# Performance work log

Hardware: AMD Instinct MI355X
Metric: run time of the kernel (lower is better)

## Reference

```python
import jax, jax.numpy as jnp
import numpy as np

DIM = 512
HEAD_DIM = 32
NUM_HEADS = DIM // HEAD_DIM
SCALE = HEAD_DIM ** -0.5
SPARSE_WINDOW = 64
LN_EPS = 1e-5


def setup_inputs() -> dict:
    key = jax.random.key(0)
    ks = jax.random.split(key, 7)
    B, S = 2, 2048
    x = jax.random.normal(ks[0], (B, S, DIM), dtype=jnp.float32)
    # parameters (Linear weights stored as [in, out] for x @ W)
    W_qkv = jax.random.normal(ks[1], (DIM, 2 * DIM), dtype=jnp.float32) * (DIM ** -0.5)
    b_qkv = jnp.zeros((2 * DIM,), dtype=jnp.float32)
    W_out = jax.random.normal(ks[2], (DIM, DIM), dtype=jnp.float32) * (DIM ** -0.5)
    b_out = jnp.zeros((DIM,), dtype=jnp.float32)
    ln_gamma = jnp.ones((DIM,), dtype=jnp.float32)
    ln_beta = jnp.zeros((DIM,), dtype=jnp.float32)
    return {"x": x, "W_qkv": W_qkv, "b_qkv": b_qkv, "W_out": W_out,
            "b_out": b_out, "ln_gamma": ln_gamma, "ln_beta": ln_beta}


def _attn(x, W_qkv, b_qkv, W_out, b_out, ln_gamma, ln_beta):
    B, S, _ = x.shape
    qkv = x @ W_qkv + b_qkv                        # [B,S,2*DIM]
    qk, v = qkv[..., :DIM], qkv[..., DIM:]
    q = jax.nn.silu(qk) * SCALE                    # shared-projection nonlinear Q
    k = jnp.tanh(qk)                               # shared-projection nonlinear K
    q = q.reshape(B, S, NUM_HEADS, HEAD_DIM)
    k = k.reshape(B, S, NUM_HEADS, HEAD_DIM)
    v = v.reshape(B, S, NUM_HEADS, HEAD_DIM)
    scores = jnp.einsum('bihd,bjhd->bhij', q, k)   # [B,H,S,S]
    # sparse window: MULTIPLICATIVE zeroing outside |i-j|<=w (faithful to source)
    i = jnp.arange(S)
    band = (jnp.abs(i[:, None] - i[None, :]) <= SPARSE_WINDOW).astype(scores.dtype)
    scores = scores * band                         # zeros still enter softmax as exp(0)
    probs = jax.nn.softmax(scores, axis=-1)
    out = jnp.einsum('bhij,bjhd->bihd', probs, v).reshape(B, S, DIM)
    out = out @ W_out + b_out
    y = x + out                                    # residual (dropout is eval no-op)
    mu = jnp.mean(y, axis=-1, keepdims=True)
    var = jnp.var(y, axis=-1, keepdims=True)
    return (y - mu) * jax.lax.rsqrt(var + LN_EPS) * ln_gamma + ln_beta


def reference(x, W_qkv, b_qkv, W_out, b_out, ln_gamma, ln_beta):
    return _attn(x, W_qkv, b_qkv, W_out, b_out, ln_gamma, ln_beta)
```

## Files before the change

### kernel.cpp

```cpp
#include <hip/hip_runtime.h>
#include <cstdint>
#include <cstddef>

#define DIMX 512
#define HDIM 32
#define NHEADS 16
#define SEQ 2048
#define BATCH 2
#define MTOT (BATCH*SEQ)
#define WIN 64
#define QSCALE 0.17677669529663687f

typedef __bf16 bf16x8 __attribute__((ext_vector_type(8)));
typedef float f32x4 __attribute__((ext_vector_type(4)));

__device__ __forceinline__ unsigned short f2bf(float f){
  unsigned u = __builtin_bit_cast(unsigned, f);
  u += 0x7FFFu + ((u >> 16) & 1u);
  return (unsigned short)(u >> 16);
}
__device__ __forceinline__ float bf2f(unsigned short s){
  return __builtin_bit_cast(float, ((unsigned)s) << 16);
}
__device__ __forceinline__ unsigned pk(float a, float b){
  return (unsigned)f2bf(a) | ((unsigned)f2bf(b) << 16);
}

__device__ __forceinline__ void gl_lds16(const void* g, void* l){
  __builtin_amdgcn_global_load_lds(
      (const __attribute__((address_space(1))) unsigned*)g,
      (__attribute__((address_space(3))) unsigned*)(unsigned)(unsigned long long)l,
      16, 0, 0);
}

template<int N> __device__ __forceinline__ void vmwait(){
  if      constexpr (N ==  8) asm volatile("s_waitcnt vmcnt(8)"  ::: "memory");
  else if constexpr (N ==  4) asm volatile("s_waitcnt vmcnt(4)"  ::: "memory");
  else                        asm volatile("s_waitcnt vmcnt(0)"  ::: "memory");
}

__global__ void k_prep(const float* __restrict__ x, unsigned short* __restrict__ xb,
                       const float* __restrict__ Wq, unsigned short* __restrict__ Wqt,
                       const float* __restrict__ Wo, unsigned short* __restrict__ Wot){
  int bx = blockIdx.x;
  if (bx < 1024){
    int i = bx * 256 + threadIdx.x;
    const float4* p = (const float4*)x + (size_t)i * 2;
    float4 a = p[0], b = p[1];
    uint4 o;
    o.x = pk(a.x, a.y); o.y = pk(a.z, a.w);
    o.z = pk(b.x, b.y); o.w = pk(b.z, b.w);
    ((uint4*)xb)[i] = o;
    return;
  }
  __shared__ float tile[32][33];
  int i = bx - 1024;
  int bxx = i % 48, byy = i / 48;
  const float* W; unsigned short* Wt; int N, n0;
  if (bxx < 32){ W = Wq; Wt = Wqt; N = 1024; n0 = bxx * 32; }
  else         { W = Wo; Wt = Wot; N = 512;  n0 = (bxx - 32) * 32; }
  int k0 = byy * 32;
  int tx = threadIdx.x & 31, ty = threadIdx.x >> 5;
  #pragma unroll
  for (int r = 0; r < 32; r += 8)
    tile[ty + r][tx] = W[(size_t)(k0 + ty + r) * N + n0 + tx];
  __syncthreads();
  #pragma unroll
  for (int r = 0; r < 32; r += 8)
    Wt[(size_t)(n0 + ty + r) * 512 + k0 + tx] = f2bf(tile[tx][ty + r]);
}

template<int MODE, int BM, int BN, int NBN>
__launch_bounds__(256)
__global__ void k_gemm(const unsigned short* __restrict__ A,
                       const unsigned short* __restrict__ Bt,
                       const float* __restrict__ bias,
                       unsigned short* __restrict__ qb,
                       unsigned short* __restrict__ kb,
                       unsigned short* __restrict__ vt,
                       float* __restrict__ vsum_p,
                       const unsigned short* __restrict__ xb,
                       unsigned short* __restrict__ yb)
{
  const int K = 512;
  constexpr int NWG = (MTOT / BM) * NBN;
  constexpr int MF  = BM / 32, NF = BN / 32;
  constexpr int LPS = (BM + BN) / 32;
  __shared__ __align__(16) unsigned short lds[2][(BM + BN) * 64];
  int tid = threadIdx.x;
  int wid = tid >> 6, lane = tid & 63;
  int wm = wid >> 1, wn = wid & 1;
  int lane15 = lane & 15, laneh = lane >> 4;

  int g = blockIdx.x;
  int gwi = (g & 7) * (NWG / 8) + (g >> 3);
  int bm = gwi / NBN, bn = gwi % NBN;

  f32x4 acc[MF][NF] = {};

  int srow_off = lane >> 3;
  int spos     = lane & 7;

  auto STAGE = [&](int buf, int kt){
    int k0 = kt * 64;
    #pragma unroll
    for (int c = 0; c < MF; ++c){
      int cidx = wid * MF + c;
      int r = cidx * 8 + srow_off;
      int ch = spos ^ (r & 7);
      gl_lds16(A + (size_t)(bm * BM + r) * K + k0 + ch * 8, &lds[buf][cidx * 512]);
    }
    #pragma unroll
    for (int c = 0; c < NF; ++c){
      int cidx = wid * NF + c;
      int r = cidx * 8 + srow_off;
      int ch = spos ^ (r & 7);
      gl_lds16(Bt + (size_t)(bn * BN + r) * K + k0 + ch * 8, &lds[buf][BM * 64 + cidx * 512]);
    }
  };

  auto COMPUTE = [&](int buf){
    #pragma unroll
    for (int kh = 0; kh < 2; ++kh){
      int chunk = kh * 4 + laneh;
      bf16x8 af[MF], bfv[NF];
      #pragma unroll
      for (int mi = 0; mi < MF; ++mi){
        int row = wm * (BM / 2) + mi * 16 + lane15;
        af[mi] = *(const bf16x8*)&lds[buf][row * 64 + (chunk ^ (row & 7)) * 8];
      }
      #pragma unroll
      for (int ni = 0; ni < NF; ++ni){
        int row = wn * (BN / 2) + ni * 16 + lane15;
        bfv[ni] = *(const bf16x8*)&lds[buf][BM * 64 + row * 64 + (chunk ^ (row & 7)) * 8];
      }
      #pragma unroll
      for (int mi = 0; mi < MF; ++mi)
        #pragma unroll
        for (int ni = 0; ni < NF; ++ni)
          acc[mi][ni] = __builtin_amdgcn_mfma_f32_16x16x32_bf16(af[mi], bfv[ni], acc[mi][ni], 0, 0, 0);
    }
  };

  STAGE(0, 0);
  #pragma unroll
  for (int kt = 0; kt < 8; ++kt){
    if (kt < 7) STAGE((kt + 1) & 1, kt + 1);
    if (kt < 7) vmwait<LPS>(); else vmwait<0>();
    __builtin_amdgcn_s_barrier();
    __builtin_amdgcn_sched_barrier(0);
    COMPUTE(kt & 1);
    __builtin_amdgcn_s_barrier();
    __builtin_amdgcn_sched_barrier(0);
  }

  if (MODE == 0 && bn >= 4){
    unsigned short (*tp)[136] = (unsigned short (*)[136])&lds[0][0];
    #pragma unroll
    for (int mi = 0; mi < MF; ++mi)
      #pragma unroll
      for (int ni = 0; ni < NF; ++ni)
        #pragma unroll
        for (int r = 0; r < 4; ++r){
          int ml = wm * (BM / 2) + mi * 16 + laneh * 4 + r;
          int nl = wn * (BN / 2) + ni * 16 + lane15;
          tp[nl][ml] = f2bf(acc[mi][ni][r] + bias[bn * BN + nl]);
        }
    __syncthreads();
    int nl = tid >> 1, half = tid & 1;
    int h = (bn - 4) * 4 + (nl >> 5), d = nl & 31;
    int b = bm >> 4, sc = bm & 15;
    int bh = b * 16 + h;
    uint4 v4[8];
    float ssum = 0.f;
    #pragma unroll
    for (int p = 0; p < 8; ++p){
      v4[p] = *(const uint4*)&tp[nl][half * 64 + p * 8];
      const unsigned* w = (const unsigned*)&v4[p];
      #pragma unroll
      for (int j = 0; j < 4; ++j)
        ssum += bf2f((unsigned short)(w[j] & 0xffff)) + bf2f((unsigned short)(w[j] >> 16));
    }
    ssum += __shfl_xor(ssum, 1);
    size_t vtoff = (size_t)(bh * HDIM + d) * SEQ + sc * 128 + half * 64;
    #pragma unroll
    for (int p = 0; p < 8; ++p) *(uint4*)(vt + vtoff + p * 8) = v4[p];
    if (half == 0) vsum_p[(sc * 32 + bh) * HDIM + d] = ssum;
  } else {
    #pragma unroll
    for (int mi = 0; mi < MF; ++mi){
      #pragma unroll
      for (int ni = 0; ni < NF; ++ni){
        #pragma unroll
        for (int r = 0; r < 4; ++r){
          int m = bm * BM + wm * (BM / 2) + mi * 16 + laneh * 4 + r;
          int nloc = wn * (BN / 2) + ni * 16 + lane15;
          int n = bn * BN + nloc;
          float val = acc[mi][ni][r] + bias[n];
          if (MODE == 0){
            int b = m >> 11, s = m & 2047;
            int h = n >> 5, d = n & 31;
            size_t idx = ((size_t)(b * 16 + h) * SEQ + s) * HDIM + d;
            float sv = val / (1.0f + __expf(-val)) * QSCALE;
            float tv = 1.0f - 2.0f / (1.0f + __expf(2.0f * val));
            qb[idx] = f2bf(sv);
            kb[idx] = f2bf(tv);
          } else {
            size_t idx = (size_t)m * DIMX + n;
            yb[idx] = f2bf(val + bf2f(xb[idx]));
          }
        }
      }
    }
  }
}

__launch_bounds__(256)
__global__ void k_attn(const unsigned short* __restrict__ qb,
                       const unsigned short* __restrict__ kb,
                       const unsigned short* __restrict__ vt,
                       const float* __restrict__ vsum_p,
                       unsigned short* __restrict__ ao)
{
  __shared__ unsigned short p_lds[4][16][40];
  int tid = threadIdx.x, wid = tid >> 6, lane = tid & 63;
  int lane15 = lane & 15, laneh = lane >> 4;
  int bh = blockIdx.y, b = bh >> 4, h = bh & 15;
  int s0 = blockIdx.x * 64 + wid * 16;

  bf16x8 qf = *(const bf16x8*)(qb + ((size_t)bh * SEQ + s0 + lane15) * HDIM + laneh * 8);
  float vs0 = 0.f, vs1 = 0.f;
  #pragma unroll
  for (int c = 0; c < 16; ++c){
    vs0 += vsum_p[(c * 32 + bh) * HDIM + lane15];
    vs1 += vsum_p[(c * 32 + bh) * HDIM + 16 + lane15];
  }

  f32x4 accv[2] = {};
  float dsum[4] = {0.f, 0.f, 0.f, 0.f};

  for (int jt = 0; jt < 9; ++jt){
    int j0 = s0 - 64 + jt * 16;
    int jc = min(max(j0 + lane15, 0), SEQ - 1);
    bf16x8 kf = *(const bf16x8*)(kb + ((size_t)bh * SEQ + jc) * HDIM + laneh * 8);
    f32x4 z = {0.f, 0.f, 0.f, 0.f};
    f32x4 sv = __builtin_amdgcn_mfma_f32_16x16x32_bf16(qf, kf, z, 0, 0, 0);
    #pragma unroll
    for (int r = 0; r < 4; ++r){
      int i = s0 + laneh * 4 + r;
      int j = j0 + lane15;
      int dj = i - j;
      bool inb = (dj <= WIN) && (dj >= -WIN) && (j >= 0) && (j < SEQ);
      float w = inb ? (__expf(sv[r]) - 1.0f) : 0.0f;
      dsum[r] += w;
      p_lds[wid][laneh * 4 + r][(jt & 1) * 16 + lane15] = f2bf(w);
    }
    if (jt & 1){
      int jc0 = j0 - 16;
      bf16x8 pa = *(const bf16x8*)&p_lds[wid][lane15][laneh * 8];
      int jv = min(max(jc0 + laneh * 8, 0), SEQ - 8);
      bf16x8 v0 = *(const bf16x8*)(vt + (size_t)(bh * HDIM + lane15) * SEQ + jv);
      bf16x8 v1 = *(const bf16x8*)(vt + (size_t)(bh * HDIM + 16 + lane15) * SEQ + jv);
      accv[0] = __builtin_amdgcn_mfma_f32_16x16x32_bf16(pa, v0, accv[0], 0, 0, 0);
      accv[1] = __builtin_amdgcn_mfma_f32_16x16x32_bf16(pa, v1, accv[1], 0, 0, 0);
    }
  }
  {
    #pragma unroll
    for (int r = 0; r < 4; ++r)
      p_lds[wid][laneh * 4 + r][16 + lane15] = 0;
    int jc0 = s0 + 64;
    bf16x8 pa = *(const bf16x8*)&p_lds[wid][lane15][laneh * 8];
    int jv = min(max(jc0 + laneh * 8, 0), SEQ - 8);
    bf16x8 v0 = *(const bf16x8*)(vt + (size_t)(bh * HDIM + lane15) * SEQ + jv);
    bf16x8 v1 = *(const bf16x8*)(vt + (size_t)(bh * HDIM + 16 + lane15) * SEQ + jv);
    accv[0] = __builtin_amdgcn_mfma_f32_16x16x32_bf16(pa, v0, accv[0], 0, 0, 0);
    accv[1] = __builtin_amdgcn_mfma_f32_16x16x32_bf16(pa, v1, accv[1], 0, 0, 0);
  }

  #pragma unroll
  for (int r = 0; r < 4; ++r){
    float v = dsum[r];
    v += __shfl_xor(v, 1); v += __shfl_xor(v, 2);
    v += __shfl_xor(v, 4); v += __shfl_xor(v, 8);
    dsum[r] = v;
  }
  #pragma unroll
  for (int r = 0; r < 4; ++r){
    int i = s0 + laneh * 4 + r;
    float dn = (float)SEQ + dsum[r];
    float o0 = (accv[0][r] + vs0) / dn;
    float o1 = (accv[1][r] + vs1) / dn;
    size_t base = (size_t)(b * SEQ + i) * DIMX + h * HDIM;
    ao[base + lane15]      = f2bf(o0);
    ao[base + 16 + lane15] = f2bf(o1);
  }
}

__global__ void k_ln(const unsigned short* __restrict__ yb, const float* __restrict__ gamma,
                     const float* __restrict__ beta, float* __restrict__ out){
  int wid = threadIdx.x >> 6, lane = threadIdx.x & 63;
  int row = blockIdx.x * 4 + wid;
  uint4 u = *(const uint4*)(yb + (size_t)row * DIMX + lane * 8);
  const unsigned* w = (const unsigned*)&u;
  float v[8];
  #pragma unroll
  for (int j = 0; j < 4; ++j){
    v[2*j]   = bf2f((unsigned short)(w[j] & 0xffff));
    v[2*j+1] = bf2f((unsigned short)(w[j] >> 16));
  }
  float s = 0.f, ss = 0.f;
  #pragma unroll
  for (int j = 0; j < 8; ++j){ s += v[j]; ss += v[j] * v[j]; }
  #pragma unroll
  for (int m = 1; m < 64; m <<= 1){ s += __shfl_xor(s, m); ss += __shfl_xor(ss, m); }
  float mu = s * (1.f / DIMX);
  float var = ss * (1.f / DIMX) - mu * mu;
  float inv = rsqrtf(var + 1e-5f);
  float4 g0 = *(const float4*)(gamma + lane * 8);
  float4 g1 = *(const float4*)(gamma + lane * 8 + 4);
  float4 b0 = *(const float4*)(beta + lane * 8);
  float4 b1 = *(const float4*)(beta + lane * 8 + 4);
  float4 o0, o1;
  o0.x = (v[0] - mu) * inv * g0.x + b0.x; o0.y = (v[1] - mu) * inv * g0.y + b0.y;
  o0.z = (v[2] - mu) * inv * g0.z + b0.z; o0.w = (v[3] - mu) * inv * g0.w + b0.w;
  o1.x = (v[4] - mu) * inv * g1.x + b1.x; o1.y = (v[5] - mu) * inv * g1.y + b1.y;
  o1.z = (v[6] - mu) * inv * g1.z + b1.z; o1.w = (v[7] - mu) * inv * g1.w + b1.w;
  float* op = out + (size_t)row * DIMX + lane * 8;
  *(float4*)op = o0; *(float4*)(op + 4) = o1;
}

extern "C" void kernel_launch(void* const* d_in, const int* in_sizes, int n_in,
                              void* d_out, int out_size, void* d_ws, size_t ws_size,
                              hipStream_t stream){
  const float* x      = (const float*)d_in[0];
  const float* W_qkv  = (const float*)d_in[1];
  const float* b_qkv  = (const float*)d_in[2];
  const float* W_out  = (const float*)d_in[3];
  const float* b_out  = (const float*)d_in[4];
  const float* gamma  = (const float*)d_in[5];
  const float* beta   = (const float*)d_in[6];
  float* out = (float*)d_out;

  char* ws = (char*)d_ws;
  size_t off = 0;
  auto alloc = [&](size_t bytes){ void* p = ws + off; off += (bytes + 255) & ~(size_t)255; return p; };
  unsigned short* xb  = (unsigned short*)alloc((size_t)MTOT * DIMX * 2);
  unsigned short* wqt = (unsigned short*)alloc((size_t)1024 * 512 * 2);
  unsigned short* wot = (unsigned short*)alloc((size_t)512 * 512 * 2);
  unsigned short* qb  = (unsigned short*)alloc((size_t)MTOT * DIMX * 2);
  unsigned short* kb  = (unsigned short*)alloc((size_t)MTOT * DIMX * 2);
  unsigned short* vt  = (unsigned short*)alloc((size_t)32 * HDIM * SEQ * 2);
  float*          vsm = (float*)alloc((size_t)16 * 32 * HDIM * 4);
  unsigned short* ao  = (unsigned short*)alloc((size_t)MTOT * DIMX * 2);
  unsigned short* yb  = (unsigned short*)alloc((size_t)MTOT * DIMX * 2);

  k_prep<<<1792, 256, 0, stream>>>(x, xb, W_qkv, wqt, W_out, wot);
  k_gemm<0, 128, 128, 8><<<256, 256, 0, stream>>>(xb, wqt, b_qkv, qb, kb, vt, vsm, nullptr, nullptr);
  k_attn<<<dim3(32, 32), 256, 0, stream>>>(qb, kb, vt, vsm, ao);
  k_gemm<1, 64, 64, 8><<<512, 256, 0, stream>>>(ao, wot, b_out, nullptr, nullptr, nullptr, nullptr, xb, yb);
  k_ln  <<<MTOT / 4, 256, 0, stream>>>(yb, gamma, beta, out);
}
```

Baseline: 45.03 us.

## Fuse output projection, residual add and LayerNorm into one kernel

Replaces the output-projection GEMM and the separate LayerNorm kernel with a single kernel. Each 512-thread block computes 16 full rows of ao@W_out with MFMA, stages the result in LDS, adds bias and residual, and normalizes in place. W_out is pre-packed in k_prep into the MFMA B-fragment layout so lanes load it directly from global memory without LDS staging. This drops one launch and the bf16 y round-trip through memory, at the cost of only 256 blocks, each streaming the whole W_out from L2 with no double buffering.

```diff
diff --git a/kernel.cpp b/kernel.cpp
--- a/kernel.cpp
+++ b/kernel.cpp
@@ -41,7 +41,7 @@
 
 __global__ void k_prep(const float* __restrict__ x, unsigned short* __restrict__ xb,
                        const float* __restrict__ Wq, unsigned short* __restrict__ Wqt,
-                       const float* __restrict__ Wo, unsigned short* __restrict__ Wot){
+                       const float* __restrict__ Wo, unsigned short* __restrict__ WotP){
   int bx = blockIdx.x;
   if (bx < 1024){
     int i = bx * 256 + threadIdx.x;
@@ -53,24 +53,42 @@
     ((uint4*)xb)[i] = o;
     return;
   }
-  __shared__ float tile[32][33];
-  int i = bx - 1024;
-  int bxx = i % 48, byy = i / 48;
-  const float* W; unsigned short* Wt; int N, n0;
-  if (bxx < 32){ W = Wq; Wt = Wqt; N = 1024; n0 = bxx * 32; }
-  else         { W = Wo; Wt = Wot; N = 512;  n0 = (bxx - 32) * 32; }
-  int k0 = byy * 32;
-  int tx = threadIdx.x & 31, ty = threadIdx.x >> 5;
-  #pragma unroll
-  for (int r = 0; r < 32; r += 8)
-    tile[ty + r][tx] = W[(size_t)(k0 + ty + r) * N + n0 + tx];
-  __syncthreads();
-  #pragma unroll
-  for (int r = 0; r < 32; r += 8)
-    Wt[(size_t)(n0 + ty + r) * 512 + k0 + tx] = f2bf(tile[tx][ty + r]);
-}
-
-template<int MODE, int BM, int BN, int NBN>
+  if (bx < 1536){
+    __shared__ float tile[32][33];
+    int i = bx - 1024;
+    int n0 = (i & 31) * 32, k0 = (i >> 5) * 32;
+    int tx = threadIdx.x & 31, ty = threadIdx.x >> 5;
+    #pragma unroll
+    for (int r = 0; r < 32; r += 8)
+      tile[ty + r][tx] = Wq[(size_t)(k0 + ty + r) * 1024 + n0 + tx];
+    __syncthreads();
+    #pragma unroll
+    for (int r = 0; r < 32; r += 8)
+      Wqt[(size_t)(n0 + ty + r) * 512 + k0 + tx] = f2bf(tile[tx][ty + r]);
+    return;
+  }
+  int wid = threadIdx.x >> 6, lane = threadIdx.x & 63;
+  int lane15 = lane & 15, laneh = lane >> 4;
+  int pair = (bx - 1536) * 4 + wid;
+  int nt = pair >> 3, ks = pair & 7;
+  int n = nt * 16 + lane15;
+  #pragma unroll
+  for (int kh = 0; kh < 2; ++kh){
+    int k0 = ks * 64 + kh * 32 + laneh * 8;
+    unsigned short pc[8];
+    #pragma unroll
+    for (int j = 0; j < 8; ++j)
+      pc[j] = f2bf(Wo[(size_t)(k0 + j) * 512 + n]);
+    uint4 o;
+    o.x = (unsigned)pc[0] | ((unsigned)pc[1] << 16);
+    o.y = (unsigned)pc[2] | ((unsigned)pc[3] << 16);
+    o.z = (unsigned)pc[4] | ((unsigned)pc[5] << 16);
+    o.w = (unsigned)pc[6] | ((unsigned)pc[7] << 16);
+    ((uint4*)WotP)[((size_t)(nt * 8 + ks) * 2 + kh) * 64 + lane] = o;
+  }
+}
+
+template<int BM, int BN, int NBN>
 __launch_bounds__(256)
 __global__ void k_gemm(const unsigned short* __restrict__ A,
                        const unsigned short* __restrict__ Bt,
@@ -78,9 +96,7 @@
                        unsigned short* __restrict__ qb,
                        unsigned short* __restrict__ kb,
                        unsigned short* __restrict__ vt,
-                       float* __restrict__ vsum_p,
-                       const unsigned short* __restrict__ xb,
-                       unsigned short* __restrict__ yb)
+                       float* __restrict__ vsum_p)
 {
   const int K = 512;
   constexpr int NWG = (MTOT / BM) * NBN;
@@ -154,7 +170,7 @@
     __builtin_amdgcn_sched_barrier(0);
   }
 
-  if (MODE == 0 && bn >= 4){
+  if (bn >= 4){
     unsigned short (*tp)[136] = (unsigned short (*)[136])&lds[0][0];
     #pragma unroll
     for (int mi = 0; mi < MF; ++mi)
@@ -194,21 +210,15 @@
         #pragma unroll
         for (int r = 0; r < 4; ++r){
           int m = bm * BM + wm * (BM / 2) + mi * 16 + laneh * 4 + r;
-          int nloc = wn * (BN / 2) + ni * 16 + lane15;
-          int n = bn * BN + nloc;
+          int n = bn * BN + wn * (BN / 2) + ni * 16 + lane15;
           float val = acc[mi][ni][r] + bias[n];
-          if (MODE == 0){
-            int b = m >> 11, s = m & 2047;
-            int h = n >> 5, d = n & 31;
-            size_t idx = ((size_t)(b * 16 + h) * SEQ + s) * HDIM + d;
-            float sv = val / (1.0f + __expf(-val)) * QSCALE;
-            float tv = 1.0f - 2.0f / (1.0f + __expf(2.0f * val));
-            qb[idx] = f2bf(sv);
-            kb[idx] = f2bf(tv);
-          } else {
-            size_t idx = (size_t)m * DIMX + n;
-            yb[idx] = f2bf(val + bf2f(xb[idx]));
-          }
+          int b = m >> 11, s = m & 2047;
+          int h = n >> 5, d = n & 31;
+          size_t idx = ((size_t)(b * 16 + h) * SEQ + s) * HDIM + d;
+          float sv = val / (1.0f + __expf(-val)) * QSCALE;
+          float tv = 1.0f - 2.0f / (1.0f + __expf(2.0f * val));
+          qb[idx] = f2bf(sv);
+          kb[idx] = f2bf(tv);
         }
       }
     }
@@ -297,37 +307,83 @@
   }
 }
 
-__global__ void k_ln(const unsigned short* __restrict__ yb, const float* __restrict__ gamma,
-                     const float* __restrict__ beta, float* __restrict__ out){
-  int wid = threadIdx.x >> 6, lane = threadIdx.x & 63;
-  int row = blockIdx.x * 4 + wid;
-  uint4 u = *(const uint4*)(yb + (size_t)row * DIMX + lane * 8);
-  const unsigned* w = (const unsigned*)&u;
-  float v[8];
-  #pragma unroll
-  for (int j = 0; j < 4; ++j){
-    v[2*j]   = bf2f((unsigned short)(w[j] & 0xffff));
-    v[2*j+1] = bf2f((unsigned short)(w[j] >> 16));
-  }
-  float s = 0.f, ss = 0.f;
-  #pragma unroll
-  for (int j = 0; j < 8; ++j){ s += v[j]; ss += v[j] * v[j]; }
-  #pragma unroll
-  for (int m = 1; m < 64; m <<= 1){ s += __shfl_xor(s, m); ss += __shfl_xor(ss, m); }
-  float mu = s * (1.f / DIMX);
+__launch_bounds__(512)
+__global__ void k_oln(const unsigned short* __restrict__ ao,
+                      const unsigned short* __restrict__ wotP,
+                      const float* __restrict__ bout,
+                      const unsigned short* __restrict__ xb,
+                      const float* __restrict__ gamma,
+                      const float* __restrict__ beta,
+                      float* __restrict__ out)
+{
+  __shared__ __align__(16) unsigned short asA[16 * 520];
+  __shared__ float tp[16][516];
+  int tid = threadIdx.x;
+  int wid = tid >> 6, lane = tid & 63;
+  int lane15 = lane & 15, laneh = lane >> 4;
+  int mrow0 = blockIdx.x * 16;
+
+  #pragma unroll
+  for (int c = 0; c < 2; ++c){
+    int row = wid * 2 + c;
+    gl_lds16(ao + (size_t)(mrow0 + row) * DIMX + (lane ^ (row & 7)) * 8,
+             &asA[row * 520]);
+  }
+
+  f32x4 acc[4] = {};
+  const uint4* bp = (const uint4*)wotP;
+
+  __syncthreads();
+
+  #pragma unroll
+  for (int kt = 0; kt < 8; ++kt){
+    #pragma unroll
+    for (int kh = 0; kh < 2; ++kh){
+      int ck = kt * 8 + kh * 4 + laneh;
+      bf16x8 af = *(const bf16x8*)&asA[lane15 * 520 + ((ck ^ (lane15 & 7)) * 8)];
+      #pragma unroll
+      for (int ni = 0; ni < 4; ++ni){
+        uint4 braw = bp[((size_t)((wid * 4 + ni) * 8 + kt) * 2 + kh) * 64 + lane];
+        acc[ni] = __builtin_amdgcn_mfma_f32_16x16x32_bf16(
+                     af, __builtin_bit_cast(bf16x8, braw), acc[ni], 0, 0, 0);
+      }
+    }
+  }
+
+  #pragma unroll
+  for (int ni = 0; ni < 4; ++ni){
+    int col = wid * 64 + ni * 16 + lane15;
+    float bv = bout[col];
+    #pragma unroll
+    for (int r = 0; r < 4; ++r)
+      tp[laneh * 4 + r][col] = acc[ni][r] + bv;
+  }
+  __syncthreads();
+
+  int tr = tid >> 5, seg = tid & 31;
+  const unsigned short* xr = xb + (size_t)(mrow0 + tr) * DIMX + seg * 16;
+  uint4 x0 = *(const uint4*)xr, x1 = *(const uint4*)(xr + 8);
+  unsigned xwv[8];
+  *(uint4*)&xwv[0] = x0; *(uint4*)&xwv[4] = x1;
+  float v[16], s = 0.f, ss = 0.f;
+  #pragma unroll
+  for (int j = 0; j < 16; ++j){
+    unsigned wb = xwv[j >> 1];
+    unsigned short hv = (j & 1) ? (unsigned short)(wb >> 16) : (unsigned short)(wb & 0xffff);
+    v[j] = tp[tr][seg * 16 + j] + bf2f(hv);
+    s += v[j]; ss += v[j] * v[j];
+  }
+  #pragma unroll
+  for (int m = 1; m < 32; m <<= 1){ s += __shfl_xor(s, m); ss += __shfl_xor(ss, m); }
+  float mu  = s * (1.f / DIMX);
   float var = ss * (1.f / DIMX) - mu * mu;
   float inv = rsqrtf(var + 1e-5f);
-  float4 g0 = *(const float4*)(gamma + lane * 8);
-  float4 g1 = *(const float4*)(gamma + lane * 8 + 4);
-  float4 b0 = *(const float4*)(beta + lane * 8);
-  float4 b1 = *(const float4*)(beta + lane * 8 + 4);
-  float4 o0, o1;
-  o0.x = (v[0] - mu) * inv * g0.x + b0.x; o0.y = (v[1] - mu) * inv * g0.y + b0.y;
-  o0.z = (v[2] - mu) * inv * g0.z + b0.z; o0.w = (v[3] - mu) * inv * g0.w + b0.w;
-  o1.x = (v[4] - mu) * inv * g1.x + b1.x; o1.y = (v[5] - mu) * inv * g1.y + b1.y;
-  o1.z = (v[6] - mu) * inv * g1.z + b1.z; o1.w = (v[7] - mu) * inv * g1.w + b1.w;
-  float* op = out + (size_t)row * DIMX + lane * 8;
-  *(float4*)op = o0; *(float4*)(op + 4) = o1;
+  float* op = out + (size_t)(mrow0 + tr) * DIMX + seg * 16;
+  const float* gp = gamma + seg * 16;
+  const float* bb = beta  + seg * 16;
+  #pragma unroll
+  for (int j = 0; j < 16; ++j)
+    op[j] = (v[j] - mu) * inv * gp[j] + bb[j];
 }
 
 extern "C" void kernel_launch(void* const* d_in, const int* in_sizes, int n_in,
@@ -345,19 +401,17 @@
   char* ws = (char*)d_ws;
   size_t off = 0;
   auto alloc = [&](size_t bytes){ void* p = ws + off; off += (bytes + 255) & ~(size_t)255; return p; };
-  unsigned short* xb  = (unsigned short*)alloc((size_t)MTOT * DIMX * 2);
-  unsigned short* wqt = (unsigned short*)alloc((size_t)1024 * 512 * 2);
-  unsigned short* wot = (unsigned short*)alloc((size_t)512 * 512 * 2);
-  unsigned short* qb  = (unsigned short*)alloc((size_t)MTOT * DIMX * 2);
-  unsigned short* kb  = (unsigned short*)alloc((size_t)MTOT * DIMX * 2);
-  unsigned short* vt  = (unsigned short*)alloc((size_t)32 * HDIM * SEQ * 2);
-  float*          vsm = (float*)alloc((size_t)16 * 32 * HDIM * 4);
-  unsigned short* ao  = (unsigned short*)alloc((size_t)MTOT * DIMX * 2);
-  unsigned short* yb  = (unsigned short*)alloc((size_t)MTOT * DIMX * 2);
-
-  k_prep<<<1792, 256, 0, stream>>>(x, xb, W_qkv, wqt, W_out, wot);
-  k_gemm<0, 128, 128, 8><<<256, 256, 0, stream>>>(xb, wqt, b_qkv, qb, kb, vt, vsm, nullptr, nullptr);
+  unsigned short* xb   = (unsigned short*)alloc((size_t)MTOT * DIMX * 2);
+  unsigned short* wqt  = (unsigned short*)alloc((size_t)1024 * 512 * 2);
+  unsigned short* wotP = (unsigned short*)alloc((size_t)512 * 512 * 2);
+  unsigned short* qb   = (unsigned short*)alloc((size_t)MTOT * DIMX * 2);
+  unsigned short* kb   = (unsigned short*)alloc((size_t)MTOT * DIMX * 2);
+  unsigned short* vt   = (unsigned short*)alloc((size_t)32 * HDIM * SEQ * 2);
+  float*          vsm  = (float*)alloc((size_t)16 * 32 * HDIM * 4);
+  unsigned short* ao   = (unsigned short*)alloc((size_t)MTOT * DIMX * 2);
+
+  k_prep<<<1600, 256, 0, stream>>>(x, xb, W_qkv, wqt, W_out, wotP);
+  k_gemm<128, 128, 8><<<256, 256, 0, stream>>>(xb, wqt, b_qkv, qb, kb, vt, vsm);
   k_attn<<<dim3(32, 32), 256, 0, stream>>>(qb, kb, vt, vsm, ao);
-  k_gemm<1, 64, 64, 8><<<512, 256, 0, stream>>>(ao, wot, b_out, nullptr, nullptr, nullptr, nullptr, xb, yb);
-  k_ln  <<<MTOT / 4, 256, 0, stream>>>(yb, gamma, beta, out);
-}
+  k_oln <<<256, 512, 0, stream>>>(ao, wotP, b_out, xb, gamma, beta, out);
+}
```

After: 48.32 us. 7.3% more time.
